# Optimization experiments

Measured on AMD Instinct MI355X. Metric: run time of the kernel, lower is better.

Reference implementation:

```python
import jax, jax.numpy as jnp
import numpy as np

N_CHAINS, L, N, D, K, H, FF = 8192, 128, 100000, 256, 8, 4, 1024
LN_EPS = 1e-5  # torch LayerNorm default
EPS = 1e-8     # module eps for mean-pool denom


def _ln(x, g, b):
    mu = jnp.mean(x, axis=-1, keepdims=True)
    var = jnp.mean((x - mu) ** 2, axis=-1, keepdims=True)
    return (x - mu) * jax.lax.rsqrt(var + LN_EPS) * g + b


def setup_inputs() -> dict:
    key = jax.random.key(0)
    ks = jax.random.split(key, 24)
    s = 1.0 / np.sqrt(D)
    inp = {
        "v": jax.random.normal(ks[0], (N, D), jnp.float32),
        "batch_idx": jax.random.randint(ks[1], (N_CHAINS, L), 0, N),
        "mask": jax.random.uniform(ks[2], (N_CHAINS, L)) > 0.5,
        "count": jax.random.randint(ks[3], (N_CHAINS,), 0, 128).astype(jnp.float32),
        "rank_scores": jax.random.normal(ks[4], (N_CHAINS, L), jnp.float32),
        "pos_embed": jnp.zeros((1, K, D), jnp.float32),
        "w_qkv": jax.random.normal(ks[5], (3 * D, D), jnp.float32) * s,
        "b_qkv": jnp.zeros((3 * D,), jnp.float32),
        "w_o": jax.random.normal(ks[6], (D, D), jnp.float32) * s,
        "b_o": jnp.zeros((D,), jnp.float32),
        "ln1_g": jnp.ones((D,), jnp.float32),
        "ln1_b": jnp.zeros((D,), jnp.float32),
        "ln2_g": jnp.ones((D,), jnp.float32),
        "ln2_b": jnp.zeros((D,), jnp.float32),
        "w_ff1": jax.random.normal(ks[7], (FF, D), jnp.float32) * s,
        "b_ff1": jnp.zeros((FF,), jnp.float32),
        "w_ff2": jax.random.normal(ks[8], (D, FF), jnp.float32) / np.sqrt(FF),
        "b_ff2": jnp.zeros((D,), jnp.float32),
        "w_out1": jax.random.normal(ks[9], (FF, D + 1), jnp.float32) * s,
        "b_out1": jnp.zeros((FF,), jnp.float32),
        "w_out2": jax.random.normal(ks[10], (D, FF), jnp.float32) / np.sqrt(FF),
        "b_out2": jnp.zeros((D,), jnp.float32),
    }
    return inp


def reference(v, batch_idx, mask, count, rank_scores, pos_embed, w_qkv, b_qkv,
              w_o, b_o, ln1_g, ln1_b, ln2_g, ln2_b, w_ff1, b_ff1, w_ff2, b_ff2,
              w_out1, b_out1, w_out2, b_out2):
    neg = jnp.finfo(jnp.float32).min
    # --- top-k relevance selection among masked positions ---
    masked_scores = jnp.where(mask, rank_scores.astype(jnp.float32), neg)
    _, top_idx = jax.lax.top_k(masked_scores, K)                # [n, K]
    picked = jnp.take_along_axis(mask, top_idx, axis=1)
    sortable = jnp.where(picked, top_idx, L)                     # sentinel L
    sortable = jnp.sort(sortable, axis=1)
    picked = sortable < L
    safe_idx = jnp.where(picked, sortable, 0)                    # [n, K]
    # gather-pack: v[batch_idx][safe_idx] == v[batch_idx gathered at safe_idx]
    member_idx = jnp.take_along_axis(batch_idx, safe_idx, axis=1)
    packed = v[member_idx] * picked[..., None].astype(v.dtype)   # [n, K, D]

    x = packed + pos_embed[:, :K, :]
    kpm = ~picked                                                # True = pad
    empty = jnp.all(kpm, axis=1)
    kpm = kpm.at[:, 0].set(jnp.where(empty, False, kpm[:, 0]))

    # --- one pre-LN transformer encoder layer (gelu, dropout=0) ---
    dh = D // H
    h = _ln(x, ln1_g, ln1_b)
    qkv = h @ w_qkv.T + b_qkv                                    # [n, K, 3D]
    q, k, val = jnp.split(qkv, 3, axis=-1)
    q = q.reshape(-1, K, H, dh)
    k = k.reshape(-1, K, H, dh)
    val = val.reshape(-1, K, H, dh)
    scores = jnp.einsum('bqhd,bkhd->bhqk', q, k) / np.sqrt(dh)
    scores = jnp.where(kpm[:, None, None, :], neg, scores)
    attn = jax.nn.softmax(scores, axis=-1)
    o = jnp.einsum('bhqk,bkhd->bqhd', attn, val).reshape(-1, K, D)
    x = x + (o @ w_o.T + b_o)
    h = _ln(x, ln2_g, ln2_b)
    x = x + jax.nn.gelu(h @ w_ff1.T + b_ff1, approximate=False) @ w_ff2.T + b_ff2

    # --- masked mean pool + log-count feature + MLP head ---
    pf = picked.astype(x.dtype)
    denom = jnp.clip(jnp.sum(pf, axis=1, keepdims=True), EPS, None)
    pooled = jnp.sum(x * pf[..., None], axis=1) / denom
    pooled = jnp.where(jnp.any(picked, axis=1, keepdims=True), pooled, 0.0)
    feat = jnp.concatenate([pooled, jnp.log1p(count.astype(x.dtype))[:, None]], axis=-1)
    return jax.nn.gelu(feat @ w_out1.T + b_out1, approximate=False) @ w_out2.T + b_out2
```

## Files before the change

kernel.cpp:

```cpp
#include <hip/hip_runtime.h>


#define DIM   256
#define LSEQ  128
#define KTOK  8

typedef __bf16 bf16x8 __attribute__((ext_vector_type(8)));
typedef float  f32x4  __attribute__((ext_vector_type(4)));
typedef unsigned short u16x8 __attribute__((ext_vector_type(8)));

__device__ __forceinline__ f32x4 mfma16(bf16x8 a, bf16x8 b, f32x4 c) {
  return __builtin_amdgcn_mfma_f32_16x16x32_bf16(a, b, c, 0, 0, 0);
}

__device__ __forceinline__ unsigned short f2bf(float f) {
  unsigned u = __float_as_uint(f);
  u = (u + 0x7FFFu + ((u >> 16) & 1u)) >> 16;
  return (unsigned short)u;
}

__device__ __forceinline__ unsigned pack2bf(float a, float b) {
  return (unsigned)f2bf(a) | ((unsigned)f2bf(b) << 16);
}

__device__ __forceinline__ float gelu_fast(float x) {
  const float y = 0.7978845608f * __builtin_fmaf(0.044715f * x * x, x, x);
  const float e = __expf(2.f * y);
  const float t = 1.f - 2.f * __builtin_amdgcn_rcpf(e + 1.f);
  return 0.5f * x * (1.f + t);
}

union U4 { unsigned u[4]; bf16x8 v; };

__device__ __forceinline__ void gload16(const unsigned short* g, unsigned short* lds_uniform) {
  auto gp = reinterpret_cast<const __attribute__((address_space(1))) unsigned*>(
      reinterpret_cast<uintptr_t>(g));
  auto lp = reinterpret_cast<__attribute__((address_space(3))) unsigned*>(
      (unsigned)reinterpret_cast<uintptr_t>(lds_uniform));
  __builtin_amdgcn_global_load_lds(gp, lp, 16, 0, 0);
}

struct Stage32 { u16x8 r[4]; };
__device__ __forceinline__ void stage_load(Stage32& st, const unsigned short* __restrict__ g, int tid) {
  #pragma unroll
  for (int i = 0; i < 4; ++i) st.r[i] = *(const u16x8*)&g[(tid + i * 512) * 8];
}
__device__ __forceinline__ void stage_commit(const Stage32& st, unsigned short* l, int tid) {
  #pragma unroll
  for (int i = 0; i < 4; ++i) *(u16x8*)&l[(tid + i * 512) * 8] = st.r[i];
}

__device__ __forceinline__ void pack_region(
    const float* __restrict__ src, unsigned short* __restrict__ dst,
    int g, int KC, int Ksrc, int Klim)
{
  const int ln = g & 63;
  const int t = g >> 6;
  const int s = t % KC;
  const int ntile = t / KC;
  const int row = ntile * 16 + (ln & 15);
  const int c0 = s * 32 + (ln >> 4) * 8;
  u16x8 o;
  #pragma unroll
  for (int j = 0; j < 8; ++j) {
    float val = (c0 + j < Klim) ? src[(long)row * Ksrc + c0 + j] : 0.f;
    o[j] = f2bf(val);
  }
  *(u16x8*)&dst[(long)g * 8] = o;
}

__device__ __forceinline__ void pack_region_kmaj(
    const float* __restrict__ src, unsigned short* __restrict__ dst,
    int g, int NT, int Ksrc)
{
  const int ln = g & 63;
  const int t = g >> 6;
  const int ntile = t % NT;
  const int s = t / NT;
  const int row = ntile * 16 + (ln & 15);
  const int c0 = s * 32 + (ln >> 4) * 8;
  u16x8 o;
  #pragma unroll
  for (int j = 0; j < 8; ++j) o[j] = f2bf(src[(long)row * Ksrc + c0 + j]);
  *(u16x8*)&dst[(long)g * 8] = o;
}

#define PREP_GROUPS 172032
__global__ __launch_bounds__(256) void k_prep(
    const float* __restrict__ wqkv, const float* __restrict__ wo,
    const float* __restrict__ wff1, const float* __restrict__ wff2,
    const float* __restrict__ wout1, const float* __restrict__ wout2,
    unsigned short* __restrict__ oq, unsigned short* __restrict__ oo,
    unsigned short* __restrict__ of1, unsigned short* __restrict__ of2,
    unsigned short* __restrict__ oo1, unsigned short* __restrict__ oo2)
{
  int g = blockIdx.x * 256 + threadIdx.x;
  if (g < 24576) { pack_region(wqkv, oq, g, 8, 256, 256); return; }
  g -= 24576;
  if (g < 8192)  { pack_region(wo, oo, g, 8, 256, 256); return; }
  g -= 8192;
  if (g < 32768) { pack_region(wff1, of1, g, 8, 256, 256); return; }
  g -= 32768;
  if (g < 32768) { pack_region_kmaj(wff2, of2, g, 16, 1024); return; }
  g -= 32768;
  if (g < 40960) { pack_region(wout1, oo1, g, 10, 257, 257); return; }
  g -= 40960;
  if (g < 32768) { pack_region_kmaj(wout2, oo2, g, 16, 1024); }
}

__global__ __launch_bounds__(256) void k_sel(
    const float* __restrict__ v, const int* __restrict__ batch_idx,
    const int* __restrict__ mask, const float* __restrict__ rank_scores,
    const float* __restrict__ pos_embed,
    const float* __restrict__ ln1g, const float* __restrict__ ln1b,
    float* __restrict__ X, unsigned short* __restrict__ H1p,
    int* __restrict__ NPICK)
{
  const int c = blockIdx.x;
  const int tid = threadIdx.x;
  __shared__ int s_mem[KTOK];
  __shared__ int s_np;

  if (tid < 64) {
    const int l = tid;
    unsigned long long key[2];
    #pragma unroll
    for (int t = 0; t < 2; ++t) {
      int p = l + 64 * t;
      int mk = mask[c * LSEQ + p];
      float s = rank_scores[c * LSEQ + p];
      unsigned u = __float_as_uint(s);
      u = (u & 0x80000000u) ? ~u : (u | 0x80000000u);
      unsigned long long kk =
          ((unsigned long long)u << 32) | (unsigned long long)(0xFFFFFFFFu - (unsigned)p);
      key[t] = mk ? kk : 0ull;
    }
    int w[KTOK];
    #pragma unroll
    for (int r = 0; r < KTOK; ++r) w[r] = 0x7FFFFFFF;
    int np = 0;
    for (int r = 0; r < KTOK; ++r) {
      unsigned long long best = key[0] > key[1] ? key[0] : key[1];
      for (int off = 32; off > 0; off >>= 1) {
        unsigned long long o = __shfl_xor(best, off, 64);
        if (o > best) best = o;
      }
      if (best == 0ull) break;
      int idx = (int)(0xFFFFFFFFu - (unsigned)(best & 0xFFFFFFFFull));
      w[np++] = idx;
      if (key[0] == best) key[0] = 0ull;
      if (key[1] == best) key[1] = 0ull;
    }
    #pragma unroll
    for (int a = 0; a < KTOK - 1; ++a)
      #pragma unroll
      for (int b2 = 0; b2 < KTOK - 1 - a; ++b2) {
        int x0 = w[b2], x1 = w[b2 + 1];
        w[b2] = min(x0, x1); w[b2 + 1] = max(x0, x1);
      }
    if (l < KTOK) s_mem[l] = (l < np) ? batch_idx[c * LSEQ + w[l]] : -1;
    if (l == 0) { s_np = np; NPICK[c] = np; }
  }
  __syncthreads();

  const int np = s_np;
  const int j = tid >> 5, q = tid & 31;
  const int r = s_mem[j];
  const float4* v4  = (const float4*)v;
  const float4* pe4 = (const float4*)pos_embed;
  float4* X4 = (float4*)X;

  float4 xv[2];
  #pragma unroll
  for (int rep = 0; rep < 2; ++rep) {
    const int f = 2 * q + rep;
    float4 pe = pe4[j * 64 + f];
    float4 val = make_float4(0.f, 0.f, 0.f, 0.f);
    if (j < np) val = v4[(long)r * 64 + f];
    xv[rep].x = val.x + pe.x; xv[rep].y = val.y + pe.y;
    xv[rep].z = val.z + pe.z; xv[rep].w = val.w + pe.w;
    X4[((long)c * KTOK + j) * 64 + f] = xv[rep];
  }
  float sum = 0.f, ss = 0.f;
  #pragma unroll
  for (int rep = 0; rep < 2; ++rep) {
    sum += xv[rep].x + xv[rep].y + xv[rep].z + xv[rep].w;
    ss  += xv[rep].x * xv[rep].x + xv[rep].y * xv[rep].y
         + xv[rep].z * xv[rep].z + xv[rep].w * xv[rep].w;
  }
  #pragma unroll
  for (int off = 1; off <= 16; off <<= 1) {
    sum += __shfl_xor(sum, off); ss += __shfl_xor(ss, off);
  }
  const float mu = sum * (1.f / 256.f);
  const float var = ss * (1.f / 256.f) - mu * mu;
  const float rstd = rsqrtf(var + 1e-5f);
  const int t = c * KTOK + j;
  const int mtile = t >> 4, lr = t & 15;
  const int s = q >> 2, lq = q & 3;
  u16x8 o;
  const int col = q * 8;
  o[0] = f2bf((xv[0].x - mu) * rstd * ln1g[col + 0] + ln1b[col + 0]);
  o[1] = f2bf((xv[0].y - mu) * rstd * ln1g[col + 1] + ln1b[col + 1]);
  o[2] = f2bf((xv[0].z - mu) * rstd * ln1g[col + 2] + ln1b[col + 2]);
  o[3] = f2bf((xv[0].w - mu) * rstd * ln1g[col + 3] + ln1b[col + 3]);
  o[4] = f2bf((xv[1].x - mu) * rstd * ln1g[col + 4] + ln1b[col + 4]);
  o[5] = f2bf((xv[1].y - mu) * rstd * ln1g[col + 5] + ln1b[col + 5]);
  o[6] = f2bf((xv[1].z - mu) * rstd * ln1g[col + 6] + ln1b[col + 6]);
  o[7] = f2bf((xv[1].w - mu) * rstd * ln1g[col + 7] + ln1b[col + 7]);
  *(u16x8*)&H1p[((long)(mtile * 8 + s) * 64 + lq * 16 + lr) * 8] = o;
}

__global__ __launch_bounds__(512, 4) void k_qkv(
    const unsigned short* __restrict__ H1p, unsigned short* __restrict__ QKVp,
    const unsigned short* __restrict__ wqp, const float* __restrict__ bqkv)
{
  __shared__ unsigned short buf[16384];
  __shared__ unsigned short sT[8 * 16 * 72];
  const int tid = threadIdx.x;
  const int wv = tid >> 6, ln = tid & 63;
  const int lr = ln & 15, lq = ln >> 4;
  const int mtile = blockIdx.x * 8 + wv;
  const f32x4 vzero = {0.f, 0.f, 0.f, 0.f};
  unsigned short* sTw = &sT[wv * 1152];

  bf16x8 af[8];
  #pragma unroll
  for (int s = 0; s < 8; ++s)
    af[s] = *(const bf16x8*)&H1p[((long)(mtile * 8 + s) * 64 + ln) * 8];

  Stage32 st;
  stage_load(st, wqp, tid);
  for (int c = 0; c < 12; ++c) {
    stage_commit(st, buf, tid);
    __syncthreads();
    if (c < 11) stage_load(st, wqp + (c + 1) * 16384, tid);
    f32x4 acc[4];
    #pragma unroll
    for (int nt = 0; nt < 4; ++nt) acc[nt] = vzero;
    #pragma unroll
    for (int s = 0; s < 8; ++s) {
      #pragma unroll
      for (int nt = 0; nt < 4; ++nt) {
        bf16x8 b = *(const bf16x8*)&buf[(nt * 8 + s) * 512 + ln * 8];
        acc[nt] = mfma16(af[s], b, acc[nt]);
      }
    }
    #pragma unroll
    for (int nt = 0; nt < 4; ++nt) {
      const float bias = bqkv[c * 64 + nt * 16 + lr];
      #pragma unroll
      for (int reg = 0; reg < 4; ++reg)
        sTw[(lq * 4 + reg) * 72 + nt * 16 + lr] = f2bf(acc[nt][reg] + bias);
    }
    const int r8 = ln >> 3, cg = ln & 7;
    #pragma unroll
    for (int h = 0; h < 2; ++h) {
      const int tok = h * 8 + r8;
      u16x8 vv = *(const u16x8*)&sTw[tok * 72 + cg * 8];
      *(u16x8*)&QKVp[((long)(mtile * 16 + tok)) * 768 + c * 64 + cg * 8] = vv;
    }
    __syncthreads();
  }
}

#define SKV 520

__global__ __launch_bounds__(128) void k_attn(
    const unsigned short* __restrict__ QKVp, const int* __restrict__ NPICK,
    unsigned short* __restrict__ Op)
{
  __shared__ unsigned short sKV[32 * SKV];
  __shared__ int s_np[4];
  const int tid = threadIdx.x;
  const int blk = blockIdx.x;
  if (tid < 4) s_np[tid] = NPICK[blk * 4 + tid];
  for (int i = tid; i < 2048; i += 128) {
    const int r = i >> 6, u = i & 63;
    *(u16x8*)&sKV[r * SKV + u * 8] =
        *(const u16x8*)&QKVp[((long)blk * 32 + r) * 768 + 256 + u * 8];
  }
  const int c = tid >> 5, hh = (tid >> 3) & 3, qi = tid & 7;
  const int qrow = c * 8 + qi;
  bf16x8 qv[8];
  #pragma unroll
  for (int dc = 0; dc < 8; ++dc)
    qv[dc] = *(const bf16x8*)&QKVp[((long)blk * 32 + qrow) * 768 + hh * 64 + dc * 8];
  __syncthreads();

  const int natt = max(1, s_np[c]);
  float sc[8];
  #pragma unroll
  for (int j = 0; j < 8; ++j) sc[j] = -1e30f;
  for (int j = 0; j < natt; ++j) {
    float d = 0.f;
    #pragma unroll
    for (int dc = 0; dc < 8; ++dc) {
      bf16x8 kv = *(const bf16x8*)&sKV[(c * 8 + j) * SKV + hh * 64 + dc * 8];
      #pragma unroll
      for (int e = 0; e < 8; ++e) d += (float)qv[dc][e] * (float)kv[e];
    }
    sc[j] = d * 0.125f;
  }
  float mx = -1e30f;
  #pragma unroll
  for (int j = 0; j < 8; ++j) mx = fmaxf(mx, sc[j]);
  float pr[8]; float ssum = 0.f;
  #pragma unroll
  for (int j = 0; j < 8; ++j) {
    float e = (j < natt) ? __expf(sc[j] - mx) : 0.f;
    pr[j] = e; ssum += e;
  }
  const float inv = 1.f / ssum;
  const int t = blk * 32 + qrow;
  const int mt = t >> 4, lrt = t & 15;
  #pragma unroll
  for (int dc = 0; dc < 8; ++dc) {
    float o8[8] = {0.f,0.f,0.f,0.f,0.f,0.f,0.f,0.f};
    for (int j = 0; j < natt; ++j) {
      const float pj = pr[j] * inv;
      bf16x8 vv = *(const bf16x8*)&sKV[(c * 8 + j) * SKV + 256 + hh * 64 + dc * 8];
      #pragma unroll
      for (int e = 0; e < 8; ++e) o8[e] += pj * (float)vv[e];
    }
    u16x8 o;
    #pragma unroll
    for (int e = 0; e < 8; ++e) o[e] = f2bf(o8[e]);
    const int s = hh * 2 + (dc >> 2), lqt = dc & 3;
    *(u16x8*)&Op[((long)(mt * 8 + s) * 64 + lqt * 16 + lrt) * 8] = o;
  }
}

__global__ __launch_bounds__(512, 4) void k_oproj(
    const unsigned short* __restrict__ Op, float* __restrict__ X,
    const unsigned short* __restrict__ wop, const float* __restrict__ bo,
    const float* __restrict__ ln2g, const float* __restrict__ ln2b,
    unsigned short* __restrict__ H2p)
{
  __shared__ unsigned short buf[16384];
  __shared__ float sTf[8 * 16 * 68];
  const int tid = threadIdx.x;
  const int wv = tid >> 6, ln = tid & 63;
  const int lr = ln & 15, lq = ln >> 4;
  const int mtile = blockIdx.x * 8 + wv;
  const f32x4 vzero = {0.f, 0.f, 0.f, 0.f};
  float* sTw = &sTf[wv * 1088];

  bf16x8 af[8];
  #pragma unroll
  for (int s = 0; s < 8; ++s)
    af[s] = *(const bf16x8*)&Op[((long)(mtile * 8 + s) * 64 + ln) * 8];

  const int r4 = ln >> 2, g4 = ln & 3;
  float lsum = 0.f, lss = 0.f;

  Stage32 st;
  stage_load(st, wop, tid);
  for (int c = 0; c < 4; ++c) {
    stage_commit(st, buf, tid);
    __syncthreads();
    if (c < 3) stage_load(st, wop + (c + 1) * 16384, tid);
    f32x4 acc[4];
    #pragma unroll
    for (int nt = 0; nt < 4; ++nt) acc[nt] = vzero;
    #pragma unroll
    for (int s = 0; s < 8; ++s) {
      #pragma unroll
      for (int nt = 0; nt < 4; ++nt) {
        bf16x8 b = *(const bf16x8*)&buf[(nt * 8 + s) * 512 + ln * 8];
        acc[nt] = mfma16(af[s], b, acc[nt]);
      }
    }
    #pragma unroll
    for (int nt = 0; nt < 4; ++nt) {
      const float bias = bo[c * 64 + nt * 16 + lr];
      #pragma unroll
      for (int reg = 0; reg < 4; ++reg)
        sTw[(lq * 4 + reg) * 68 + nt * 16 + lr] = acc[nt][reg] + bias;
    }
    #pragma unroll
    for (int it = 0; it < 4; ++it) {
      const int gi = it * 4 + g4;
      f32x4 vv = *(const f32x4*)&sTw[r4 * 68 + gi * 4];
      float4* xp = (float4*)&X[((long)(mtile * 16 + r4)) * DIM + c * 64 + gi * 4];
      float4 old = *xp;
      old.x += vv[0]; old.y += vv[1]; old.z += vv[2]; old.w += vv[3];
      *xp = old;
      lsum += old.x + old.y + old.z + old.w;
      lss  += old.x * old.x + old.y * old.y + old.z * old.z + old.w * old.w;
    }
    __syncthreads();
  }
  lsum += __shfl_xor(lsum, 1); lss += __shfl_xor(lss, 1);
  lsum += __shfl_xor(lsum, 2); lss += __shfl_xor(lss, 2);
  const float mu = lsum * (1.f / 256.f);
  const float rstd = rsqrtf(lss * (1.f / 256.f) - mu * mu + 1e-5f);
  const int row = mtile * 16 + r4;
  #pragma unroll
  for (int i = 0; i < 8; ++i) {
    const int q = i * 4 + g4;
    const float4 x0 = *(const float4*)&X[(long)row * DIM + q * 8];
    const float4 x1 = *(const float4*)&X[(long)row * DIM + q * 8 + 4];
    const float4 g0 = *(const float4*)&ln2g[q * 8];
    const float4 g1 = *(const float4*)&ln2g[q * 8 + 4];
    const float4 b0 = *(const float4*)&ln2b[q * 8];
    const float4 b1 = *(const float4*)&ln2b[q * 8 + 4];
    u16x8 o;
    o[0] = f2bf((x0.x - mu) * rstd * g0.x + b0.x);
    o[1] = f2bf((x0.y - mu) * rstd * g0.y + b0.y);
    o[2] = f2bf((x0.z - mu) * rstd * g0.z + b0.z);
    o[3] = f2bf((x0.w - mu) * rstd * g0.w + b0.w);
    o[4] = f2bf((x1.x - mu) * rstd * g1.x + b1.x);
    o[5] = f2bf((x1.y - mu) * rstd * g1.y + b1.y);
    o[6] = f2bf((x1.z - mu) * rstd * g1.z + b1.z);
    o[7] = f2bf((x1.w - mu) * rstd * g1.w + b1.w);
    *(u16x8*)&H2p[((long)(mtile * 8 + (q >> 2)) * 64 + (q & 3) * 16 + r4) * 8] = o;
  }
}

__global__ __launch_bounds__(512, 4) void k_ff(
    const float* __restrict__ X, const unsigned short* __restrict__ H2p,
    const unsigned short* __restrict__ w1p, const unsigned short* __restrict__ w2p,
    const float* __restrict__ bff1, const float* __restrict__ bff2,
    const int* __restrict__ NPICK, const float* __restrict__ count,
    unsigned short* __restrict__ Fp)
{
  __shared__ unsigned short bufA[16384];
  __shared__ unsigned short bufB[16384];
  const int tid = threadIdx.x;
  const int wv = tid >> 6, ln = tid & 63;
  const int lr = ln & 15, lq = ln >> 4;
  const int mtile = blockIdx.x * 8 + wv;
  const f32x4 vzero = {0.f, 0.f, 0.f, 0.f};

  const int chain0 = mtile * 2;
  const int npc = NPICK[chain0 + (lq >> 1)];
  float mk[4];
  #pragma unroll
  for (int reg = 0; reg < 4; ++reg)
    mk[reg] = (((lq * 4 + reg) & 7) < npc) ? 1.f : 0.f;

  float pooled[16];
  #pragma unroll
  for (int nt = 0; nt < 16; ++nt) pooled[nt] = 0.f;

  const int laneA = ((lq & 1) * 2) * 16 + lr;
  const int laneB = laneA + 16;
  const bool hi = (lq & 2) != 0;

  #pragma unroll
  for (int i = 0; i < 4; ++i) {
    const int off = (i * 512 + wv * 64) * 8;
    gload16(w1p + off + ln * 8, &bufA[off]);
  }
  __syncthreads();

  for (int f = 0; f < 16; ++f) {
    #pragma unroll
    for (int i = 0; i < 4; ++i) {
      const int off = (i * 512 + wv * 64) * 8;
      gload16(w2p + (long)f * 16384 + off + ln * 8, &bufB[off]);
    }

    f32x4 ga[4];
    #pragma unroll
    for (int nt = 0; nt < 4; ++nt) ga[nt] = vzero;
    #pragma unroll
    for (int s = 0; s < 8; ++s) {
      const bf16x8 afs = *(const bf16x8*)&H2p[((long)(mtile * 8 + s) * 64 + ln) * 8];
      #pragma unroll
      for (int nt = 0; nt < 4; ++nt) {
        bf16x8 w1f = *(const bf16x8*)&bufA[(nt * 8 + s) * 512 + ln * 8];
        ga[nt] = mfma16(w1f, afs, ga[nt]);
      }
    }
    unsigned p0[4], p1[4];
    #pragma unroll
    for (int nt = 0; nt < 4; ++nt) {
      const float4 b4 = *(const float4*)&bff1[f * 64 + nt * 16 + lq * 4];
      const float g0 = gelu_fast(ga[nt][0] + b4.x);
      const float g1 = gelu_fast(ga[nt][1] + b4.y);
      const float g2 = gelu_fast(ga[nt][2] + b4.z);
      const float g3 = gelu_fast(ga[nt][3] + b4.w);
      p0[nt] = pack2bf(g0, g1);
      p1[nt] = pack2bf(g2, g3);
    }
    __syncthreads();

    if (f < 15) {
      #pragma unroll
      for (int i = 0; i < 4; ++i) {
        const int off = (i * 512 + wv * 64) * 8;
        gload16(w1p + (long)(f + 1) * 16384 + off + ln * 8, &bufA[off]);
      }
    }

    f32x4 t[16];
    #pragma unroll
    for (int nt = 0; nt < 16; ++nt) t[nt] = vzero;
    #pragma unroll
    for (int s2 = 0; s2 < 2; ++s2) {
      const unsigned a0 = (unsigned)__shfl((int)p0[2 * s2],     laneA, 64);
      const unsigned a1 = (unsigned)__shfl((int)p1[2 * s2],     laneA, 64);
      const unsigned a2 = (unsigned)__shfl((int)p0[2 * s2],     laneB, 64);
      const unsigned a3 = (unsigned)__shfl((int)p1[2 * s2],     laneB, 64);
      const unsigned c0 = (unsigned)__shfl((int)p0[2 * s2 + 1], laneA, 64);
      const unsigned c1 = (unsigned)__shfl((int)p1[2 * s2 + 1], laneA, 64);
      const unsigned c2 = (unsigned)__shfl((int)p0[2 * s2 + 1], laneB, 64);
      const unsigned c3 = (unsigned)__shfl((int)p1[2 * s2 + 1], laneB, 64);
      U4 uu;
      uu.u[0] = hi ? c0 : a0; uu.u[1] = hi ? c1 : a1;
      uu.u[2] = hi ? c2 : a2; uu.u[3] = hi ? c3 : a3;
      const bf16x8 gfrag = uu.v;
      #pragma unroll
      for (int nt = 0; nt < 16; ++nt) {
        bf16x8 w2f = *(const bf16x8*)&bufB[(s2 * 16 + nt) * 512 + ln * 8];
        t[nt] = mfma16(gfrag, w2f, t[nt]);
      }
    }
    #pragma unroll
    for (int nt = 0; nt < 16; ++nt) {
      pooled[nt] += mk[0] * t[nt][0] + mk[1] * t[nt][1]
                  + mk[2] * t[nt][2] + mk[3] * t[nt][3];
    }
    __syncthreads();
  }

  float psum[16];
  #pragma unroll
  for (int nt = 0; nt < 16; ++nt) {
    const int col = nt * 16 + lr;
    const float bias = bff2[col];
    float ps = pooled[nt];
    #pragma unroll
    for (int reg = 0; reg < 4; ++reg) {
      const int row = lq * 4 + reg;
      ps += mk[reg] * (X[((long)mtile * 16 + row) * DIM + col] + bias);
    }
    psum[nt] = ps;
  }
  const float inv = (npc > 0) ? (1.f / (float)npc) : 0.f;
  #pragma unroll
  for (int nt = 0; nt < 16; ++nt) {
    psum[nt] += __shfl_xor(psum[nt], 16);
    psum[nt] *= inv;
  }
  if ((lq & 1) == 0) {
    const int ch = chain0 + (lq >> 1);
    const int rtile = ch >> 4, lrf = ch & 15;
    #pragma unroll
    for (int nt = 0; nt < 16; ++nt) {
      const int col = nt * 16 + lr;
      const int s = col >> 5, lqf = (col >> 3) & 3, j = col & 7;
      Fp[((long)(rtile * 10 + s) * 64 + lqf * 16 + lrf) * 8 + j] = f2bf(psum[nt]);
    }
  } else if (lr < 8) {
    const int ch = chain0 + (lq >> 1);
    const int rtile = ch >> 4, lrf = ch & 15;
    const int q = 32 + lr;
    const int s = q >> 2, lqf = q & 3;
    u16x8 o = {0,0,0,0,0,0,0,0};
    if (q == 32) o[0] = f2bf(log1pf(count[ch]));
    *(u16x8*)&Fp[((long)(rtile * 10 + s) * 64 + lqf * 16 + lrf) * 8] = o;
  }
}

__global__ __launch_bounds__(512, 4) void k_headmlp(
    const unsigned short* __restrict__ Fp,
    const unsigned short* __restrict__ wo1p, const unsigned short* __restrict__ wo2p,
    const float* __restrict__ bout1, const float* __restrict__ bout2,
    float* __restrict__ out)
{
  __shared__ unsigned short bufA[20480];
  __shared__ unsigned short bufB[16384];
  const int tid = threadIdx.x;
  const int fq = blockIdx.x & 3;
  const int mchunk = blockIdx.x >> 2;
  const int wv = tid >> 6, ln = tid & 63;
  const int lr = ln & 15, lq = ln >> 4;
  const int rtile = mchunk * 8 + wv;
  const f32x4 vzero = {0.f, 0.f, 0.f, 0.f};

  f32x4 oacc[16];
  #pragma unroll
  for (int nt = 0; nt < 16; ++nt) oacc[nt] = vzero;

  const int laneA = ((lq & 1) * 2) * 16 + lr;
  const int laneB = laneA + 16;
  const bool hi = (lq & 2) != 0;

  for (int it = 0; it < 4; ++it) {
    const int f = fq * 4 + it;
    __syncthreads();
    #pragma unroll
    for (int i = 0; i < 5; ++i) {
      const int off = (i * 512 + wv * 64) * 8;
      gload16(wo1p + (long)f * 20480 + off + ln * 8, &bufA[off]);
    }
    #pragma unroll
    for (int i = 0; i < 4; ++i) {
      const int off = (i * 512 + wv * 64) * 8;
      gload16(wo2p + (long)f * 16384 + off + ln * 8, &bufB[off]);
    }
    __syncthreads();

    f32x4 ga[4];
    #pragma unroll
    for (int nt = 0; nt < 4; ++nt) ga[nt] = vzero;
    #pragma unroll
    for (int s = 0; s < 10; ++s) {
      const bf16x8 afs = *(const bf16x8*)&Fp[((long)(rtile * 10 + s) * 64 + ln) * 8];
      #pragma unroll
      for (int nt = 0; nt < 4; ++nt) {
        bf16x8 w1f = *(const bf16x8*)&bufA[(nt * 10 + s) * 512 + ln * 8];
        ga[nt] = mfma16(w1f, afs, ga[nt]);
      }
    }
    unsigned p0[4], p1[4];
    #pragma unroll
    for (int nt = 0; nt < 4; ++nt) {
      const float4 b4 = *(const float4*)&bout1[f * 64 + nt * 16 + lq * 4];
      const float g0 = gelu_fast(ga[nt][0] + b4.x);
      const float g1 = gelu_fast(ga[nt][1] + b4.y);
      const float g2 = gelu_fast(ga[nt][2] + b4.z);
      const float g3 = gelu_fast(ga[nt][3] + b4.w);
      p0[nt] = pack2bf(g0, g1);
      p1[nt] = pack2bf(g2, g3);
    }
    #pragma unroll
    for (int s2 = 0; s2 < 2; ++s2) {
      const unsigned a0 = (unsigned)__shfl((int)p0[2 * s2],     laneA, 64);
      const unsigned a1 = (unsigned)__shfl((int)p1[2 * s2],     laneA, 64);
      const unsigned a2 = (unsigned)__shfl((int)p0[2 * s2],     laneB, 64);
      const unsigned a3 = (unsigned)__shfl((int)p1[2 * s2],     laneB, 64);
      const unsigned c0 = (unsigned)__shfl((int)p0[2 * s2 + 1], laneA, 64);
      const unsigned c1 = (unsigned)__shfl((int)p1[2 * s2 + 1], laneA, 64);
      const unsigned c2 = (unsigned)__shfl((int)p0[2 * s2 + 1], laneB, 64);
      const unsigned c3 = (unsigned)__shfl((int)p1[2 * s2 + 1], laneB, 64);
      U4 uu;
      uu.u[0] = hi ? c0 : a0; uu.u[1] = hi ? c1 : a1;
      uu.u[2] = hi ? c2 : a2; uu.u[3] = hi ? c3 : a3;
      const bf16x8 gfrag = uu.v;
      #pragma unroll
      for (int nt = 0; nt < 16; ++nt) {
        bf16x8 w2f = *(const bf16x8*)&bufB[(s2 * 16 + nt) * 512 + ln * 8];
        oacc[nt] = mfma16(gfrag, w2f, oacc[nt]);
      }
    }
  }
  #pragma unroll
  for (int nt = 0; nt < 16; ++nt) {
    const int col = nt * 16 + lr;
    const float bias = (fq == 0) ? bout2[col] : 0.f;
    #pragma unroll
    for (int reg = 0; reg < 4; ++reg) {
      const int row = mchunk * 128 + wv * 16 + lq * 4 + reg;
      atomicAdd(&out[(long)row * DIM + col], oacc[nt][reg] + bias);
    }
  }
}

extern "C" void kernel_launch(void* const* d_in, const int* in_sizes, int n_in,
                              void* d_out, int out_size, void* d_ws, size_t ws_size,
                              hipStream_t stream) {
  (void)in_sizes; (void)n_in; (void)out_size; (void)ws_size;
  const float* v          = (const float*)d_in[0];
  const int*   batch_idx  = (const int*)  d_in[1];
  const int*   mask       = (const int*)  d_in[2];
  const float* count      = (const float*)d_in[3];
  const float* rank       = (const float*)d_in[4];
  const float* pe         = (const float*)d_in[5];
  const float* w_qkv      = (const float*)d_in[6];
  const float* b_qkv      = (const float*)d_in[7];
  const float* w_o        = (const float*)d_in[8];
  const float* b_o        = (const float*)d_in[9];
  const float* ln1g       = (const float*)d_in[10];
  const float* ln1b       = (const float*)d_in[11];
  const float* ln2g       = (const float*)d_in[12];
  const float* ln2b       = (const float*)d_in[13];
  const float* w_ff1      = (const float*)d_in[14];
  const float* b_ff1      = (const float*)d_in[15];
  const float* w_ff2      = (const float*)d_in[16];
  const float* b_ff2      = (const float*)d_in[17];
  const float* w_out1     = (const float*)d_in[18];
  const float* b_out1     = (const float*)d_in[19];
  const float* w_out2     = (const float*)d_in[20];
  const float* b_out2     = (const float*)d_in[21];
  float* out = (float*)d_out;

  char* ws = (char*)d_ws;
  float*          X     = (float*)ws;
  unsigned short* H1p   = (unsigned short*)(ws + 67108864);
  unsigned short* Op    = H1p;
  unsigned short* QKVp  = (unsigned short*)(ws + 100663296);
  unsigned short* H2p   = QKVp;
  unsigned short* Fp    = (unsigned short*)(ws + 134217728);
  int*            NPICK = (int*)(ws + 201326592);
  unsigned short* wq_bf   = (unsigned short*)(ws + 201359360);
  unsigned short* wo_bf   = (unsigned short*)(ws + 201752576);
  unsigned short* wff1_bf = (unsigned short*)(ws + 201883648);
  unsigned short* wff2_bf = (unsigned short*)(ws + 202407936);
  unsigned short* wo1_bf  = (unsigned short*)(ws + 202932224);
  unsigned short* wo2_bf  = (unsigned short*)(ws + 203587584);

  k_prep<<<PREP_GROUPS / 256, 256, 0, stream>>>(
      w_qkv, w_o, w_ff1, w_ff2, w_out1, w_out2,
      wq_bf, wo_bf, wff1_bf, wff2_bf, wo1_bf, wo2_bf);

  k_sel<<<8192, 256, 0, stream>>>(v, batch_idx, mask, rank, pe,
                                  ln1g, ln1b, X, H1p, NPICK);

  k_qkv<<<512, 512, 0, stream>>>(H1p, QKVp, wq_bf, b_qkv);

  k_attn<<<2048, 128, 0, stream>>>(QKVp, NPICK, Op);

  k_oproj<<<512, 512, 0, stream>>>(Op, X, wo_bf, b_o, ln2g, ln2b, H2p);

  k_ff<<<512, 512, 0, stream>>>(X, H2p, wff1_bf, wff2_bf, b_ff1, b_ff2,
                                NPICK, count, Fp);

  hipMemsetAsync(out, 0, (size_t)8192 * 256 * sizeof(float), stream);

  k_headmlp<<<256, 512, 0, stream>>>(Fp, wo1_bf, wo2_bf, b_out1, b_out2, out);
}
```

Measured before the change: 586.1 us.

## Process two M-tiles per wave in FF kernel to reuse LDS weight fragments

```diff
diff --git a/kernel.cpp b/kernel.cpp
--- a/kernel.cpp
+++ b/kernel.cpp
@@ -418,114 +418,30 @@
   }
 }
 
-__global__ __launch_bounds__(512, 4) void k_ff(
-    const float* __restrict__ X, const unsigned short* __restrict__ H2p,
-    const unsigned short* __restrict__ w1p, const unsigned short* __restrict__ w2p,
-    const float* __restrict__ bff1, const float* __restrict__ bff2,
-    const int* __restrict__ NPICK, const float* __restrict__ count,
-    unsigned short* __restrict__ Fp)
-{
-  __shared__ unsigned short bufA[16384];
-  __shared__ unsigned short bufB[16384];
-  const int tid = threadIdx.x;
-  const int wv = tid >> 6, ln = tid & 63;
-  const int lr = ln & 15, lq = ln >> 4;
-  const int mtile = blockIdx.x * 8 + wv;
-  const f32x4 vzero = {0.f, 0.f, 0.f, 0.f};
-
-  const int chain0 = mtile * 2;
-  const int npc = NPICK[chain0 + (lq >> 1)];
-  float mk[4];
-  #pragma unroll
-  for (int reg = 0; reg < 4; ++reg)
-    mk[reg] = (((lq * 4 + reg) & 7) < npc) ? 1.f : 0.f;
-
-  float pooled[16];
-  #pragma unroll
-  for (int nt = 0; nt < 16; ++nt) pooled[nt] = 0.f;
-
-  const int laneA = ((lq & 1) * 2) * 16 + lr;
-  const int laneB = laneA + 16;
-  const bool hi = (lq & 2) != 0;
-
-  #pragma unroll
-  for (int i = 0; i < 4; ++i) {
-    const int off = (i * 512 + wv * 64) * 8;
-    gload16(w1p + off + ln * 8, &bufA[off]);
-  }
-  __syncthreads();
-
-  for (int f = 0; f < 16; ++f) {
-    #pragma unroll
-    for (int i = 0; i < 4; ++i) {
-      const int off = (i * 512 + wv * 64) * 8;
-      gload16(w2p + (long)f * 16384 + off + ln * 8, &bufB[off]);
-    }
-
-    f32x4 ga[4];
-    #pragma unroll
-    for (int nt = 0; nt < 4; ++nt) ga[nt] = vzero;
-    #pragma unroll
-    for (int s = 0; s < 8; ++s) {
-      const bf16x8 afs = *(const bf16x8*)&H2p[((long)(mtile * 8 + s) * 64 + ln) * 8];
-      #pragma unroll
-      for (int nt = 0; nt < 4; ++nt) {
-        bf16x8 w1f = *(const bf16x8*)&bufA[(nt * 8 + s) * 512 + ln * 8];
-        ga[nt] = mfma16(w1f, afs, ga[nt]);
-      }
-    }
-    unsigned p0[4], p1[4];
-    #pragma unroll
-    for (int nt = 0; nt < 4; ++nt) {
-      const float4 b4 = *(const float4*)&bff1[f * 64 + nt * 16 + lq * 4];
-      const float g0 = gelu_fast(ga[nt][0] + b4.x);
-      const float g1 = gelu_fast(ga[nt][1] + b4.y);
-      const float g2 = gelu_fast(ga[nt][2] + b4.z);
-      const float g3 = gelu_fast(ga[nt][3] + b4.w);
-      p0[nt] = pack2bf(g0, g1);
-      p1[nt] = pack2bf(g2, g3);
-    }
-    __syncthreads();
-
-    if (f < 15) {
-      #pragma unroll
-      for (int i = 0; i < 4; ++i) {
-        const int off = (i * 512 + wv * 64) * 8;
-        gload16(w1p + (long)(f + 1) * 16384 + off + ln * 8, &bufA[off]);
-      }
-    }
-
-    f32x4 t[16];
-    #pragma unroll
-    for (int nt = 0; nt < 16; ++nt) t[nt] = vzero;
-    #pragma unroll
-    for (int s2 = 0; s2 < 2; ++s2) {
-      const unsigned a0 = (unsigned)__shfl((int)p0[2 * s2],     laneA, 64);
-      const unsigned a1 = (unsigned)__shfl((int)p1[2 * s2],     laneA, 64);
-      const unsigned a2 = (unsigned)__shfl((int)p0[2 * s2],     laneB, 64);
-      const unsigned a3 = (unsigned)__shfl((int)p1[2 * s2],     laneB, 64);
-      const unsigned c0 = (unsigned)__shfl((int)p0[2 * s2 + 1], laneA, 64);
-      const unsigned c1 = (unsigned)__shfl((int)p1[2 * s2 + 1], laneA, 64);
-      const unsigned c2 = (unsigned)__shfl((int)p0[2 * s2 + 1], laneB, 64);
-      const unsigned c3 = (unsigned)__shfl((int)p1[2 * s2 + 1], laneB, 64);
-      U4 uu;
-      uu.u[0] = hi ? c0 : a0; uu.u[1] = hi ? c1 : a1;
-      uu.u[2] = hi ? c2 : a2; uu.u[3] = hi ? c3 : a3;
-      const bf16x8 gfrag = uu.v;
-      #pragma unroll
-      for (int nt = 0; nt < 16; ++nt) {
-        bf16x8 w2f = *(const bf16x8*)&bufB[(s2 * 16 + nt) * 512 + ln * 8];
-        t[nt] = mfma16(gfrag, w2f, t[nt]);
-      }
-    }
-    #pragma unroll
-    for (int nt = 0; nt < 16; ++nt) {
-      pooled[nt] += mk[0] * t[nt][0] + mk[1] * t[nt][1]
-                  + mk[2] * t[nt][2] + mk[3] * t[nt][3];
-    }
-    __syncthreads();
-  }
-
+__device__ __forceinline__ bf16x8 build_gfrag(
+    const unsigned* p0, const unsigned* p1, int s2,
+    int laneA, int laneB, bool hi)
+{
+  const unsigned a0 = (unsigned)__shfl((int)p0[2 * s2],     laneA, 64);
+  const unsigned a1 = (unsigned)__shfl((int)p1[2 * s2],     laneA, 64);
+  const unsigned a2 = (unsigned)__shfl((int)p0[2 * s2],     laneB, 64);
+  const unsigned a3 = (unsigned)__shfl((int)p1[2 * s2],     laneB, 64);
+  const unsigned c0 = (unsigned)__shfl((int)p0[2 * s2 + 1], laneA, 64);
+  const unsigned c1 = (unsigned)__shfl((int)p1[2 * s2 + 1], laneA, 64);
+  const unsigned c2 = (unsigned)__shfl((int)p0[2 * s2 + 1], laneB, 64);
+  const unsigned c3 = (unsigned)__shfl((int)p1[2 * s2 + 1], laneB, 64);
+  U4 uu;
+  uu.u[0] = hi ? c0 : a0; uu.u[1] = hi ? c1 : a1;
+  uu.u[2] = hi ? c2 : a2; uu.u[3] = hi ? c3 : a3;
+  return uu.v;
+}
+
+__device__ __forceinline__ void ff_pool_write(
+    const float* __restrict__ X, const float* __restrict__ bff2,
+    const float* __restrict__ count, unsigned short* __restrict__ Fp,
+    const float* pooled, const float* mk, int npc, int mtile,
+    int lq, int lr)
+{
   float psum[16];
   #pragma unroll
   for (int nt = 0; nt < 16; ++nt) {
@@ -545,6 +461,7 @@
     psum[nt] += __shfl_xor(psum[nt], 16);
     psum[nt] *= inv;
   }
+  const int chain0 = mtile * 2;
   if ((lq & 1) == 0) {
     const int ch = chain0 + (lq >> 1);
     const int rtile = ch >> 4, lrf = ch & 15;
@@ -563,6 +480,124 @@
     if (q == 32) o[0] = f2bf(log1pf(count[ch]));
     *(u16x8*)&Fp[((long)(rtile * 10 + s) * 64 + lqf * 16 + lrf) * 8] = o;
   }
+}
+
+__global__ __launch_bounds__(256, 2) void k_ff(
+    const float* __restrict__ X, const unsigned short* __restrict__ H2p,
+    const unsigned short* __restrict__ w1p, const unsigned short* __restrict__ w2p,
+    const float* __restrict__ bff1, const float* __restrict__ bff2,
+    const int* __restrict__ NPICK, const float* __restrict__ count,
+    unsigned short* __restrict__ Fp)
+{
+  __shared__ unsigned short bufA[16384];
+  __shared__ unsigned short bufB[16384];
+  const int tid = threadIdx.x;
+  const int wv = tid >> 6, ln = tid & 63;
+  const int lr = ln & 15, lq = ln >> 4;
+  const int mtA = blockIdx.x * 8 + wv * 2;
+  const int mtB = mtA + 1;
+  const f32x4 vzero = {0.f, 0.f, 0.f, 0.f};
+
+  const int npcA = NPICK[mtA * 2 + (lq >> 1)];
+  const int npcB = NPICK[mtB * 2 + (lq >> 1)];
+  float mkA[4], mkB[4];
+  #pragma unroll
+  for (int reg = 0; reg < 4; ++reg) {
+    const int r8 = (lq * 4 + reg) & 7;
+    mkA[reg] = (r8 < npcA) ? 1.f : 0.f;
+    mkB[reg] = (r8 < npcB) ? 1.f : 0.f;
+  }
+
+  float pooledA[16], pooledB[16];
+  #pragma unroll
+  for (int nt = 0; nt < 16; ++nt) { pooledA[nt] = 0.f; pooledB[nt] = 0.f; }
+
+  const int laneA = ((lq & 1) * 2) * 16 + lr;
+  const int laneB = laneA + 16;
+  const bool hi = (lq & 2) != 0;
+
+  #pragma unroll
+  for (int i = 0; i < 8; ++i) {
+    const int off = (i * 256 + wv * 64) * 8;
+    gload16(w1p + off + ln * 8, &bufA[off]);
+  }
+  __syncthreads();
+
+  for (int f = 0; f < 16; ++f) {
+    #pragma unroll
+    for (int i = 0; i < 8; ++i) {
+      const int off = (i * 256 + wv * 64) * 8;
+      gload16(w2p + (long)f * 16384 + off + ln * 8, &bufB[off]);
+    }
+
+    f32x4 gaA[4], gaB[4];
+    #pragma unroll
+    for (int nt = 0; nt < 4; ++nt) { gaA[nt] = vzero; gaB[nt] = vzero; }
+    #pragma unroll
+    for (int s = 0; s < 8; ++s) {
+      const bf16x8 afsA = *(const bf16x8*)&H2p[((long)(mtA * 8 + s) * 64 + ln) * 8];
+      const bf16x8 afsB = *(const bf16x8*)&H2p[((long)(mtB * 8 + s) * 64 + ln) * 8];
+      #pragma unroll
+      for (int nt = 0; nt < 4; ++nt) {
+        const bf16x8 w1f = *(const bf16x8*)&bufA[(nt * 8 + s) * 512 + ln * 8];
+        gaA[nt] = mfma16(w1f, afsA, gaA[nt]);
+        gaB[nt] = mfma16(w1f, afsB, gaB[nt]);
+      }
+    }
+    unsigned p0A[4], p1A[4], p0B[4], p1B[4];
+    #pragma unroll
+    for (int nt = 0; nt < 4; ++nt) {
+      const float4 b4 = *(const float4*)&bff1[f * 64 + nt * 16 + lq * 4];
+      p0A[nt] = pack2bf(gelu_fast(gaA[nt][0] + b4.x), gelu_fast(gaA[nt][1] + b4.y));
+      p1A[nt] = pack2bf(gelu_fast(gaA[nt][2] + b4.z), gelu_fast(gaA[nt][3] + b4.w));
+      p0B[nt] = pack2bf(gelu_fast(gaB[nt][0] + b4.x), gelu_fast(gaB[nt][1] + b4.y));
+      p1B[nt] = pack2bf(gelu_fast(gaB[nt][2] + b4.z), gelu_fast(gaB[nt][3] + b4.w));
+    }
+    __syncthreads();
+
+    if (f < 15) {
+      #pragma unroll
+      for (int i = 0; i < 8; ++i) {
+        const int off = (i * 256 + wv * 64) * 8;
+        gload16(w1p + (long)(f + 1) * 16384 + off + ln * 8, &bufA[off]);
+      }
+    }
+
+    bf16x8 gfA[2], gfB[2];
+    #pragma unroll
+    for (int s2 = 0; s2 < 2; ++s2) {
+      gfA[s2] = build_gfrag(p0A, p1A, s2, laneA, laneB, hi);
+      gfB[s2] = build_gfrag(p0B, p1B, s2, laneA, laneB, hi);
+    }
+
+    #pragma unroll
+    for (int nh = 0; nh < 2; ++nh) {
+      f32x4 tA[8], tB[8];
+      #pragma unroll
+      for (int nt = 0; nt < 8; ++nt) { tA[nt] = vzero; tB[nt] = vzero; }
+      #pragma unroll
+      for (int s2 = 0; s2 < 2; ++s2) {
+        #pragma unroll
+        for (int nt = 0; nt < 8; ++nt) {
+          const bf16x8 w2f =
+              *(const bf16x8*)&bufB[(s2 * 16 + nh * 8 + nt) * 512 + ln * 8];
+          tA[nt] = mfma16(gfA[s2], w2f, tA[nt]);
+          tB[nt] = mfma16(gfB[s2], w2f, tB[nt]);
+        }
+      }
+      #pragma unroll
+      for (int nt = 0; nt < 8; ++nt) {
+        pooledA[nh * 8 + nt] += mkA[0] * tA[nt][0] + mkA[1] * tA[nt][1]
+                              + mkA[2] * tA[nt][2] + mkA[3] * tA[nt][3];
+        pooledB[nh * 8 + nt] += mkB[0] * tB[nt][0] + mkB[1] * tB[nt][1]
+                              + mkB[2] * tB[nt][2] + mkB[3] * tB[nt][3];
+      }
+    }
+    __syncthreads();
+  }
+
+  ff_pool_write(X, bff2, count, Fp, pooledA, mkA, npcA, mtA, lq, lr);
+  ff_pool_write(X, bff2, count, Fp, pooledB, mkB, npcB, mtB, lq, lr);
 }
 
 __global__ __launch_bounds__(512, 4) void k_headmlp(
@@ -716,7 +751,7 @@
 
   k_oproj<<<512, 512, 0, stream>>>(Op, X, wo_bf, b_o, ln2g, ln2b, H2p);
 
-  k_ff<<<512, 512, 0, stream>>>(X, H2p, wff1_bf, wff2_bf, b_ff1, b_ff2,
+  k_ff<<<512, 256, 0, stream>>>(X, H2p, wff1_bf, wff2_bf, b_ff1, b_ff2,
                                 NPICK, count, Fp);
 
   hipMemsetAsync(out, 0, (size_t)8192 * 256 * sizeof(float), stream);
```

New measurement: 530.3 us. 9.5% less time.

## Pool GELU activations before FF2 matmul to shrink second GEMM

Applied to the files above, without the earlier changes.

```diff
diff --git a/kernel.cpp b/kernel.cpp
--- a/kernel.cpp
+++ b/kernel.cpp
@@ -14,20 +14,31 @@
 }
 
 __device__ __forceinline__ unsigned short f2bf(float f) {
-  unsigned u = __float_as_uint(f);
-  u = (u + 0x7FFFu + ((u >> 16) & 1u)) >> 16;
-  return (unsigned short)u;
+  union { __bf16 h; unsigned short u; } cv;
+  cv.h = (__bf16)f;
+  return cv.u;
 }
 
 __device__ __forceinline__ unsigned pack2bf(float a, float b) {
-  return (unsigned)f2bf(a) | ((unsigned)f2bf(b) << 16);
+  union { __bf16 h2[2]; unsigned u; } cv;
+  cv.h2[0] = (__bf16)a; cv.h2[1] = (__bf16)b;
+  return cv.u;
 }
 
 __device__ __forceinline__ float gelu_fast(float x) {
-  const float y = 0.7978845608f * __builtin_fmaf(0.044715f * x * x, x, x);
+  const float x2 = x * x;
+  const float y = x * __builtin_fmaf(0.0356774081f, x2, 0.7978845608f);
   const float e = __expf(2.f * y);
-  const float t = 1.f - 2.f * __builtin_amdgcn_rcpf(e + 1.f);
+  const float r = __builtin_amdgcn_rcpf(e + 1.f);
+  const float t = __builtin_fmaf(-2.f, r, 1.f);
   return 0.5f * x * (1.f + t);
+}
+
+__device__ __forceinline__ float rsum8(float v) {
+  v += __shfl_xor(v, 1);
+  v += __shfl_xor(v, 2);
+  v += __shfl_xor(v, 4);
+  return v;
 }
 
 union U4 { unsigned u[4]; bf16x8 v; };
@@ -418,150 +429,166 @@
   }
 }
 
-__global__ __launch_bounds__(512, 4) void k_ff(
+__global__ __launch_bounds__(256, 2) void k_ff(
     const float* __restrict__ X, const unsigned short* __restrict__ H2p,
     const unsigned short* __restrict__ w1p, const unsigned short* __restrict__ w2p,
     const float* __restrict__ bff1, const float* __restrict__ bff2,
     const int* __restrict__ NPICK, const float* __restrict__ count,
     unsigned short* __restrict__ Fp)
 {
-  __shared__ unsigned short bufA[16384];
-  __shared__ unsigned short bufB[16384];
+  __shared__ unsigned short buf[2][8192];
+  __shared__ unsigned short Gs[16384];
+  __shared__ float Pxf[4096];
   const int tid = threadIdx.x;
   const int wv = tid >> 6, ln = tid & 63;
   const int lr = ln & 15, lq = ln >> 4;
-  const int mtile = blockIdx.x * 8 + wv;
+  const int blk = blockIdx.x;
+  const int mtA = blk * 8 + wv * 2, mtB = mtA + 1;
   const f32x4 vzero = {0.f, 0.f, 0.f, 0.f};
 
-  const int chain0 = mtile * 2;
-  const int npc = NPICK[chain0 + (lq >> 1)];
-  float mk[4];
-  #pragma unroll
-  for (int reg = 0; reg < 4; ++reg)
-    mk[reg] = (((lq * 4 + reg) & 7) < npc) ? 1.f : 0.f;
-
-  float pooled[16];
-  #pragma unroll
-  for (int nt = 0; nt < 16; ++nt) pooled[nt] = 0.f;
-
-  const int laneA = ((lq & 1) * 2) * 16 + lr;
-  const int laneB = laneA + 16;
-  const bool hi = (lq & 2) != 0;
-
-  #pragma unroll
-  for (int i = 0; i < 4; ++i) {
-    const int off = (i * 512 + wv * 64) * 8;
-    gload16(w1p + off + ln * 8, &bufA[off]);
+  const int sub = (ln >> 3) & 1;
+  const int npcAl = NPICK[mtA * 2 + sub];
+  const int npcBl = NPICK[mtB * 2 + sub];
+  const float mTA = ((ln & 7) < npcAl) ? 1.f : 0.f;
+  const float mTB = ((ln & 7) < npcBl) ? 1.f : 0.f;
+  const int chA = wv * 4 + sub;
+  const int chB = wv * 4 + 2 + sub;
+
+  bf16x8 afA[8], afB[8];
+  #pragma unroll
+  for (int s = 0; s < 8; ++s) {
+    afA[s] = *(const bf16x8*)&H2p[((long)(mtA * 8 + s) * 64 + ln) * 8];
+    afB[s] = *(const bf16x8*)&H2p[((long)(mtB * 8 + s) * 64 + ln) * 8];
+  }
+
+  #pragma unroll
+  for (int c = 0; c < 4; ++c) {
+    const int off = (c * 256 + wv * 64) * 8;
+    gload16(w1p + off + ln * 8, &buf[0][off]);
   }
   __syncthreads();
 
-  for (int f = 0; f < 16; ++f) {
-    #pragma unroll
-    for (int i = 0; i < 4; ++i) {
-      const int off = (i * 512 + wv * 64) * 8;
-      gload16(w2p + (long)f * 16384 + off + ln * 8, &bufB[off]);
-    }
-
-    f32x4 ga[4];
-    #pragma unroll
-    for (int nt = 0; nt < 4; ++nt) ga[nt] = vzero;
+  for (int i = 0; i < 32; ++i) {
+    const unsigned short* bcur = buf[i & 1];
+    if (i < 31) {
+      unsigned short* bnxt = buf[(i + 1) & 1];
+      #pragma unroll
+      for (int c = 0; c < 4; ++c) {
+        const int off = (c * 256 + wv * 64) * 8;
+        gload16(w1p + (long)(i + 1) * 8192 + off + ln * 8, &bnxt[off]);
+      }
+    }
+    f32x4 gaA[2], gaB[2];
+    #pragma unroll
+    for (int nt = 0; nt < 2; ++nt) { gaA[nt] = vzero; gaB[nt] = vzero; }
     #pragma unroll
     for (int s = 0; s < 8; ++s) {
-      const bf16x8 afs = *(const bf16x8*)&H2p[((long)(mtile * 8 + s) * 64 + ln) * 8];
-      #pragma unroll
-      for (int nt = 0; nt < 4; ++nt) {
-        bf16x8 w1f = *(const bf16x8*)&bufA[(nt * 8 + s) * 512 + ln * 8];
-        ga[nt] = mfma16(w1f, afs, ga[nt]);
-      }
-    }
-    unsigned p0[4], p1[4];
-    #pragma unroll
-    for (int nt = 0; nt < 4; ++nt) {
-      const float4 b4 = *(const float4*)&bff1[f * 64 + nt * 16 + lq * 4];
-      const float g0 = gelu_fast(ga[nt][0] + b4.x);
-      const float g1 = gelu_fast(ga[nt][1] + b4.y);
-      const float g2 = gelu_fast(ga[nt][2] + b4.z);
-      const float g3 = gelu_fast(ga[nt][3] + b4.w);
-      p0[nt] = pack2bf(g0, g1);
-      p1[nt] = pack2bf(g2, g3);
+      #pragma unroll
+      for (int nt = 0; nt < 2; ++nt) {
+        const bf16x8 w1f = *(const bf16x8*)&bcur[(nt * 8 + s) * 512 + ln * 8];
+        gaA[nt] = mfma16(w1f, afA[s], gaA[nt]);
+        gaB[nt] = mfma16(w1f, afB[s], gaB[nt]);
+      }
+    }
+    float sA[2][4], sB[2][4];
+    #pragma unroll
+    for (int nt = 0; nt < 2; ++nt) {
+      const float4 b4 = *(const float4*)&bff1[i * 32 + nt * 16 + lq * 4];
+      sA[nt][0] = rsum8(gelu_fast(gaA[nt][0] + b4.x) * mTA);
+      sA[nt][1] = rsum8(gelu_fast(gaA[nt][1] + b4.y) * mTA);
+      sA[nt][2] = rsum8(gelu_fast(gaA[nt][2] + b4.z) * mTA);
+      sA[nt][3] = rsum8(gelu_fast(gaA[nt][3] + b4.w) * mTA);
+      sB[nt][0] = rsum8(gelu_fast(gaB[nt][0] + b4.x) * mTB);
+      sB[nt][1] = rsum8(gelu_fast(gaB[nt][1] + b4.y) * mTB);
+      sB[nt][2] = rsum8(gelu_fast(gaB[nt][2] + b4.z) * mTB);
+      sB[nt][3] = rsum8(gelu_fast(gaB[nt][3] + b4.w) * mTB);
+    }
+    if ((ln & 7) == 0) {
+      #pragma unroll
+      for (int nt = 0; nt < 2; ++nt)
+        #pragma unroll
+        for (int reg = 0; reg < 4; ++reg) {
+          const int r = lq * 4 + reg;
+          const int pos = (nt * 2 + (r >> 3)) * 16;
+          const int e = r & 7;
+          Gs[i * 512 + (chA + pos) * 8 + e] = f2bf(sA[nt][reg]);
+          Gs[i * 512 + (chB + pos) * 8 + e] = f2bf(sB[nt][reg]);
+        }
     }
     __syncthreads();
-
-    if (f < 15) {
-      #pragma unroll
-      for (int i = 0; i < 4; ++i) {
-        const int off = (i * 512 + wv * 64) * 8;
-        gload16(w1p + (long)(f + 1) * 16384 + off + ln * 8, &bufA[off]);
-      }
-    }
-
-    f32x4 t[16];
-    #pragma unroll
-    for (int nt = 0; nt < 16; ++nt) t[nt] = vzero;
-    #pragma unroll
-    for (int s2 = 0; s2 < 2; ++s2) {
-      const unsigned a0 = (unsigned)__shfl((int)p0[2 * s2],     laneA, 64);
-      const unsigned a1 = (unsigned)__shfl((int)p1[2 * s2],     laneA, 64);
-      const unsigned a2 = (unsigned)__shfl((int)p0[2 * s2],     laneB, 64);
-      const unsigned a3 = (unsigned)__shfl((int)p1[2 * s2],     laneB, 64);
-      const unsigned c0 = (unsigned)__shfl((int)p0[2 * s2 + 1], laneA, 64);
-      const unsigned c1 = (unsigned)__shfl((int)p1[2 * s2 + 1], laneA, 64);
-      const unsigned c2 = (unsigned)__shfl((int)p0[2 * s2 + 1], laneB, 64);
-      const unsigned c3 = (unsigned)__shfl((int)p1[2 * s2 + 1], laneB, 64);
-      U4 uu;
-      uu.u[0] = hi ? c0 : a0; uu.u[1] = hi ? c1 : a1;
-      uu.u[2] = hi ? c2 : a2; uu.u[3] = hi ? c3 : a3;
-      const bf16x8 gfrag = uu.v;
-      #pragma unroll
-      for (int nt = 0; nt < 16; ++nt) {
-        bf16x8 w2f = *(const bf16x8*)&bufB[(s2 * 16 + nt) * 512 + ln * 8];
-        t[nt] = mfma16(gfrag, w2f, t[nt]);
-      }
-    }
-    #pragma unroll
-    for (int nt = 0; nt < 16; ++nt) {
-      pooled[nt] += mk[0] * t[nt][0] + mk[1] * t[nt][1]
-                  + mk[2] * t[nt][2] + mk[3] * t[nt][3];
-    }
-    __syncthreads();
-  }
-
-  float psum[16];
-  #pragma unroll
-  for (int nt = 0; nt < 16; ++nt) {
-    const int col = nt * 16 + lr;
-    const float bias = bff2[col];
-    float ps = pooled[nt];
-    #pragma unroll
-    for (int reg = 0; reg < 4; ++reg) {
-      const int row = lq * 4 + reg;
-      ps += mk[reg] * (X[((long)mtile * 16 + row) * DIM + col] + bias);
-    }
-    psum[nt] = ps;
-  }
-  const float inv = (npc > 0) ? (1.f / (float)npc) : 0.f;
-  #pragma unroll
-  for (int nt = 0; nt < 16; ++nt) {
-    psum[nt] += __shfl_xor(psum[nt], 16);
-    psum[nt] *= inv;
-  }
-  if ((lq & 1) == 0) {
-    const int ch = chain0 + (lq >> 1);
-    const int rtile = ch >> 4, lrf = ch & 15;
+  }
+
+  #pragma unroll
+  for (int grp = 0; grp < 2; ++grp) {
+    const int mt = grp ? mtB : mtA;
+    const int npc = NPICK[mt * 2 + (lq >> 1)];
+    float mk[4];
+    #pragma unroll
+    for (int reg = 0; reg < 4; ++reg)
+      mk[reg] = (((lq * 4 + reg) & 7) < npc) ? 1.f : 0.f;
     #pragma unroll
     for (int nt = 0; nt < 16; ++nt) {
       const int col = nt * 16 + lr;
-      const int s = col >> 5, lqf = (col >> 3) & 3, j = col & 7;
-      Fp[((long)(rtile * 10 + s) * 64 + lqf * 16 + lrf) * 8 + j] = f2bf(psum[nt]);
-    }
-  } else if (lr < 8) {
-    const int ch = chain0 + (lq >> 1);
-    const int rtile = ch >> 4, lrf = ch & 15;
-    const int q = 32 + lr;
-    const int s = q >> 2, lqf = q & 3;
-    u16x8 o = {0,0,0,0,0,0,0,0};
-    if (q == 32) o[0] = f2bf(log1pf(count[ch]));
-    *(u16x8*)&Fp[((long)(rtile * 10 + s) * 64 + lqf * 16 + lrf) * 8] = o;
+      float ps = 0.f;
+      #pragma unroll
+      for (int reg = 0; reg < 4; ++reg)
+        ps += mk[reg] * X[((long)mt * 16 + lq * 4 + reg) * DIM + col];
+      ps += __shfl_xor(ps, 16);
+      if ((lq & 1) == 0)
+        Pxf[(wv * 4 + grp * 2 + (lq >> 1)) * 256 + col] = ps;
+    }
+  }
+  __syncthreads();
+
+  f32x4 C[4];
+  #pragma unroll
+  for (int nt = 0; nt < 4; ++nt) C[nt] = vzero;
+  for (int s = 0; s < 32; ++s) {
+    const bf16x8 ag = *(const bf16x8*)&Gs[s * 512 + ln * 8];
+    #pragma unroll
+    for (int nt = 0; nt < 4; ++nt) {
+      const bf16x8 w2f =
+          *(const bf16x8*)&w2p[((long)(s * 16 + wv * 4 + nt) * 64 + ln) * 8];
+      C[nt] = mfma16(ag, w2f, C[nt]);
+    }
+  }
+  #pragma unroll
+  for (int nt = 0; nt < 4; ++nt) {
+    #pragma unroll
+    for (int reg = 0; reg < 4; ++reg) {
+      const int m = lq * 4 + reg;
+      const int col = wv * 64 + nt * 16 + lr;
+      Pxf[m * 256 + col] += C[nt][reg];
+    }
+  }
+  __syncthreads();
+
+  for (int t = tid; t < 640; t += 256) {
+    const int ch = t / 40, grp = t % 40;
+    const int npc = NPICK[blk * 16 + ch];
+    u16x8 o;
+    if (grp < 32) {
+      const float inv = (npc > 0) ? (1.f / (float)npc) : 0.f;
+      const f32x4 p0 = *(const f32x4*)&Pxf[ch * 256 + grp * 8];
+      const f32x4 p1 = *(const f32x4*)&Pxf[ch * 256 + grp * 8 + 4];
+      const float4 b0 = *(const float4*)&bff2[grp * 8];
+      const float4 b1 = *(const float4*)&bff2[grp * 8 + 4];
+      if (npc > 0) {
+        o[0] = f2bf(p0[0] * inv + b0.x); o[1] = f2bf(p0[1] * inv + b0.y);
+        o[2] = f2bf(p0[2] * inv + b0.z); o[3] = f2bf(p0[3] * inv + b0.w);
+        o[4] = f2bf(p1[0] * inv + b1.x); o[5] = f2bf(p1[1] * inv + b1.y);
+        o[6] = f2bf(p1[2] * inv + b1.z); o[7] = f2bf(p1[3] * inv + b1.w);
+      } else {
+        #pragma unroll
+        for (int j = 0; j < 8; ++j) o[j] = 0;
+      }
+    } else {
+      #pragma unroll
+      for (int j = 0; j < 8; ++j) o[j] = 0;
+      if (grp == 32) o[0] = f2bf(log1pf(count[blk * 16 + ch]));
+    }
+    const int s = grp >> 2, lqf = grp & 3;
+    *(u16x8*)&Fp[((long)(blk * 10 + s) * 64 + lqf * 16 + ch) * 8] = o;
   }
 }
 
@@ -716,7 +743,7 @@
 
   k_oproj<<<512, 512, 0, stream>>>(Op, X, wo_bf, b_o, ln2g, ln2b, H2p);
 
-  k_ff<<<512, 512, 0, stream>>>(X, H2p, wff1_bf, wff2_bf, b_ff1, b_ff2,
+  k_ff<<<512, 256, 0, stream>>>(X, H2p, wff1_bf, wff2_bf, b_ff1, b_ff2,
                                 NPICK, count, Fp);
 
   hipMemsetAsync(out, 0, (size_t)8192 * 256 * sizeof(float), stream);
```

New measurement: 520.5 us. 11.2% less time.
